# Kernel optimization log

Hardware: AMD Instinct MI355X
Metric: run time of the kernel (lower is better)

The kernel has to match this reference:

```python
import jax, jax.numpy as jnp
import numpy as np
import math

EPS = 1e-5
NUM_HEADS = 16


def _ln(x, g, b):
    m = jnp.mean(x, axis=-1, keepdims=True)
    v = jnp.mean(jnp.square(x - m), axis=-1, keepdims=True)
    return (x - m) * jax.lax.rsqrt(v + EPS) * g + b


def setup_inputs() -> dict:
    key = jax.random.key(0)
    ks = jax.random.split(key, 20)
    B, S, D = 16, 256, 1024
    G, L, QL = 576, 64, 16
    V = L * QL
    s = 0.02
    inp = {
        "hidden_states": jax.random.normal(ks[0], (B, S, D), jnp.float32),
        "global_ctx": jax.random.normal(ks[1], (B, G, D), jnp.float32),
        "vision_pos": jax.random.randint(ks[2], (B, G), 0, 1000),
        "instruct_pos": jax.random.randint(ks[3], (B, L), 0, 1000),
        "queries": jax.random.normal(ks[4], (B, V, D), jnp.float32),
        "image_tokens": jax.random.normal(ks[5], (B, V, D), jnp.float32),
        "query_len": QL,
        "W_in": jax.random.normal(ks[6], (D, 2 * D), jnp.float32) * s,
        "W_ctx": jax.random.normal(ks[7], (D, D), jnp.float32) * s,
        "ln_q_g": jnp.ones((D,), jnp.float32),
        "ln_q_b": jnp.zeros((D,), jnp.float32),
        "Wq": jax.random.normal(ks[8], (D, D), jnp.float32) * s,
        "ln_k_g": jnp.ones((D,), jnp.float32),
        "ln_k_b": jnp.zeros((D,), jnp.float32),
        "Wk": jax.random.normal(ks[9], (D, D), jnp.float32) * s,
        "ln_v_g": jnp.ones((D,), jnp.float32),
        "ln_v_b": jnp.zeros((D,), jnp.float32),
        "Wv": jax.random.normal(ks[10], (D, D), jnp.float32) * s,
        "Wo": jax.random.normal(ks[11], (D, D), jnp.float32) * s,
        "norm_g": jnp.ones((D,), jnp.float32),
        "norm_b": jnp.zeros((D,), jnp.float32),
        "W1": jax.random.normal(ks[12], (D, D), jnp.float32) * s,
        "W2": jax.random.normal(ks[13], (D, D), jnp.float32) * s,
    }
    return inp


def reference(hidden_states, global_ctx, vision_pos, instruct_pos, queries,
              image_tokens, query_len, W_in, W_ctx, ln_q_g, ln_q_b, Wq,
              ln_k_g, ln_k_b, Wk, ln_v_g, ln_v_b, Wv, Wo, norm_g, norm_b,
              W1, W2):
    B, V, _ = queries.shape
    D = hidden_states.shape[-1]
    G = global_ctx.shape[1]
    L = instruct_pos.shape[1]
    H = NUM_HEADS
    hd = D // H
    scale = 1.0 / math.sqrt(hd)
    Hq = int(math.sqrt(query_len))          # query grid side
    Hgc = int(math.sqrt(G))                 # ctx grid side
    Hw = Hgc // Hq                          # window side
    Wt = Hw * Hw                            # tokens per window

    residual = image_tokens
    # proj_in on concatenated queries
    pq = jnp.concatenate([queries, image_tokens], axis=-1) @ W_in.T  # (B,V,D)

    # window extraction: (B,Hgc,Wgc,D) -> (B, query_len, Wt, D)
    win = global_ctx.reshape(B, Hq, Hw, Hq, Hw, D)
    win = win.transpose(0, 1, 3, 2, 4, 5).reshape(B, query_len, Wt, D)
    win = win @ W_ctx.T                      # proj_context, shared across L

    # cross-attention: each query v attends only to window (v mod query_len)
    q = _ln(pq, ln_q_g, ln_q_b) @ Wq.T
    q = q.reshape(B, L, query_len, H, hd)
    k = (_ln(win, ln_k_g, ln_k_b) @ Wk.T).reshape(B, query_len, Wt, H, hd)
    v = (_ln(win, ln_v_g, ln_v_b) @ Wv.T).reshape(B, query_len, Wt, H, hd)

    scores = jnp.einsum('blqhd,bqwhd->blqhw', q, k) * scale
    attn = jax.nn.softmax(scores, axis=-1)
    ao = jnp.einsum('blqhw,bqwhd->blqhd', attn, v).reshape(B, V, D)
    ao = ao @ Wo.T

    x = _ln(ao + pq, norm_g, norm_b)
    out = jax.nn.gelu(x @ W1.T, approximate=False) @ W2.T
    return out + residual
```

## Files before the change

### kernel.cpp

```cpp
#include <hip/hip_runtime.h>
#include <cstdint>
#include <cstddef>

typedef unsigned short u16;
typedef __bf16 bf16_t;
typedef bf16_t bf16x8 __attribute__((ext_vector_type(8)));
typedef float f32x4 __attribute__((ext_vector_type(4)));

#define DEV __device__ __forceinline__
#define AS1 __attribute__((address_space(1)))
#define AS3 __attribute__((address_space(3)))

DEV u16 f2bf(float f) {
  unsigned u = __float_as_uint(f);
  u += 0x7fffu + ((u >> 16) & 1u);
  return (u16)(u >> 16);
}
DEV float bf2f(u16 h) {
  return __uint_as_float(((unsigned)h) << 16);
}

struct Cvt9 {
  const float* s[9];
  u16* d[9];
  long cumv[10];
};

__global__ __launch_bounds__(256)
void convert_batch(Cvt9 jobs) {
  const long total = jobs.cumv[9];
  for (long i = (long)blockIdx.x * 256 + threadIdx.x; i < total;
       i += (long)gridDim.x * 256) {
    int j = 0;
#pragma unroll
    for (int t = 0; t < 8; ++t)
      if (i >= jobs.cumv[t + 1]) j = t + 1;
    const long e = (i - jobs.cumv[j]) * 4;
    float4 v = *(const float4*)(jobs.s[j] + e);
    ushort4 o;
    o.x = f2bf(v.x); o.y = f2bf(v.y); o.z = f2bf(v.z); o.w = f2bf(v.w);
    *(ushort4*)(jobs.d[j] + e) = o;
  }
}

__global__ __launch_bounds__(256)
void build_acat(const float* __restrict__ q, const float* __restrict__ it,
                u16* __restrict__ dst) {
  const long total = 16384l * 2048 / 4;
  for (long i = (long)blockIdx.x * 256 + threadIdx.x; i < total;
       i += (long)gridDim.x * 256) {
    long e = i * 4;
    int m = (int)(e >> 11);
    int k = (int)(e & 2047);
    const float* s = (k < 1024) ? (q + (long)m * 1024 + k)
                                : (it + (long)m * 1024 + (k - 1024));
    float4 v = *(const float4*)s;
    ushort4 o;
    o.x = f2bf(v.x); o.y = f2bf(v.y); o.z = f2bf(v.z); o.w = f2bf(v.w);
    *(ushort4*)(dst + e) = o;
  }
}

__global__ __launch_bounds__(256)
void ln_rows(const float* __restrict__ x, const float* __restrict__ g,
             const float* __restrict__ b, u16* __restrict__ out) {
  __shared__ float red[8];
  const int row = blockIdx.x, tid = threadIdx.x;
  const float* xr = x + (size_t)row * 1024;
  float4 v = *(const float4*)(xr + tid * 4);
  float s = v.x + v.y + v.z + v.w;
  float ss = v.x * v.x + v.y * v.y + v.z * v.z + v.w * v.w;
#pragma unroll
  for (int o = 32; o > 0; o >>= 1) { s += __shfl_xor(s, o); ss += __shfl_xor(ss, o); }
  if ((tid & 63) == 0) { red[tid >> 6] = s; red[4 + (tid >> 6)] = ss; }
  __syncthreads();
  s = red[0] + red[1] + red[2] + red[3];
  ss = red[4] + red[5] + red[6] + red[7];
  const float mean = s * 0.0009765625f;
  const float var = ss * 0.0009765625f - mean * mean;
  const float rinv = rsqrtf(var + 1e-5f);
  const int c = tid * 4;
  float4 gg = *(const float4*)(g + c);
  float4 bb = *(const float4*)(b + c);
  ushort4 o4;
  o4.x = f2bf((v.x - mean) * rinv * gg.x + bb.x);
  o4.y = f2bf((v.y - mean) * rinv * gg.y + bb.y);
  o4.z = f2bf((v.z - mean) * rinv * gg.z + bb.z);
  o4.w = f2bf((v.w - mean) * rinv * gg.w + bb.w);
  *(ushort4*)(out + (size_t)row * 1024 + c) = o4;
}

__global__ __launch_bounds__(256)
void ln_kv(const float* __restrict__ winp,
           const float* __restrict__ gk, const float* __restrict__ bk,
           const float* __restrict__ gv, const float* __restrict__ bv,
           u16* __restrict__ kout, u16* __restrict__ vout) {
  __shared__ float red[8];
  const int m = blockIdx.x, tid = threadIdx.x;
  const int b = m / 576, rem = m % 576;
  const int qw = rem / 36, w = rem % 36;
  const int gidx = (qw >> 2) * 144 + (w / 6) * 24 + (qw & 3) * 6 + (w % 6);
  const float* xr = winp + ((size_t)b * 576 + gidx) * 1024;
  float4 v = *(const float4*)(xr + tid * 4);
  float s = v.x + v.y + v.z + v.w;
  float ss = v.x * v.x + v.y * v.y + v.z * v.z + v.w * v.w;
#pragma unroll
  for (int o = 32; o > 0; o >>= 1) { s += __shfl_xor(s, o); ss += __shfl_xor(ss, o); }
  if ((tid & 63) == 0) { red[tid >> 6] = s; red[4 + (tid >> 6)] = ss; }
  __syncthreads();
  s = red[0] + red[1] + red[2] + red[3];
  ss = red[4] + red[5] + red[6] + red[7];
  const float mean = s * 0.0009765625f;
  const float var = ss * 0.0009765625f - mean * mean;
  const float rinv = rsqrtf(var + 1e-5f);
  const int c = tid * 4;
  float4 gg = *(const float4*)(gk + c);
  float4 bb = *(const float4*)(bk + c);
  float4 g2 = *(const float4*)(gv + c);
  float4 b2 = *(const float4*)(bv + c);
  float nx = (v.x - mean) * rinv, ny = (v.y - mean) * rinv;
  float nz = (v.z - mean) * rinv, nw = (v.w - mean) * rinv;
  ushort4 ok, ov;
  ok.x = f2bf(nx * gg.x + bb.x); ok.y = f2bf(ny * gg.y + bb.y);
  ok.z = f2bf(nz * gg.z + bb.z); ok.w = f2bf(nw * gg.w + bb.w);
  ov.x = f2bf(nx * g2.x + b2.x); ov.y = f2bf(ny * g2.y + b2.y);
  ov.z = f2bf(nz * g2.z + b2.z); ov.w = f2bf(nw * g2.w + b2.w);
  *(ushort4*)(kout + (size_t)m * 1024 + c) = ok;
  *(ushort4*)(vout + (size_t)m * 1024 + c) = ov;
}

template <int EPI>
__global__ __launch_bounds__(512, 2)
void gemm256(const u16* __restrict__ A, const u16* __restrict__ Bw,
             u16* __restrict__ outB, float* __restrict__ outF,
             const float* __restrict__ addF, int M, int N, int K) {
  __shared__ __align__(16) u16 lds[2][2][16384];
  const int tid = threadIdx.x;
  const int wave = tid >> 6, lane = tid & 63;
  const int fr = lane & 15, fq = lane >> 4;
  const int swz = (blockIdx.x & 7) * ((int)gridDim.x >> 3) + (blockIdx.x >> 3);
  const int brow = (swz >> 2) << 8;
  const int bcol = (swz & 3) << 8;

  const int srow = tid >> 3;
  const int cgo = ((tid & 7) ^ (srow & 7)) << 3;
  const u16* pa0 = A + (size_t)(brow + srow) * K + cgo;
  const u16* pb0 = Bw + (size_t)(bcol + srow) * K + cgo;
  const size_t rstep = (size_t)64 * K;

  f32x4 acc[8][4];
#pragma unroll
  for (int mf = 0; mf < 8; ++mf)
#pragma unroll
    for (int nf = 0; nf < 4; ++nf) acc[mf][nf] = (f32x4){0.f, 0.f, 0.f, 0.f};

  const int fx = fr & 7;
  const int arow = (wave >> 2) * 128 + fr;
  const int brl = (wave & 3) * 64 + fr;

  auto STAGE_A = [&](int buf, int kt) {
    const int k0 = kt << 6;
#pragma unroll
    for (int i = 0; i < 4; ++i)
      __builtin_amdgcn_global_load_lds((const AS1 void*)(pa0 + i * rstep + k0),
                                       (AS3 void*)&lds[buf][0][i * 4096 + tid * 8],
                                       16, 0, 0);
  };
  auto STAGE_B = [&](int buf, int kt) {
    const int k0 = kt << 6;
#pragma unroll
    for (int i = 0; i < 4; ++i)
      __builtin_amdgcn_global_load_lds((const AS1 void*)(pb0 + i * rstep + k0),
                                       (AS3 void*)&lds[buf][1][i * 4096 + tid * 8],
                                       16, 0, 0);
  };

  const int NT = K >> 6;
  STAGE_A(0, 0);
  STAGE_B(0, 0);
  asm volatile("s_waitcnt vmcnt(0)" ::: "memory");
  __builtin_amdgcn_s_barrier();

  bf16x8 a[4], b[4];
  for (int t = 0; t < NT; ++t) {
    const u16* la = &lds[t & 1][0][0];
    const u16* lb = &lds[t & 1][1][0];
    const int nxt = (t + 1) & 1;

#pragma unroll
    for (int nf = 0; nf < 4; ++nf)
      b[nf] = *(const bf16x8*)&lb[(brl + nf * 16) * 64 + ((fq ^ fx) << 3)];
#pragma unroll
    for (int mf = 0; mf < 4; ++mf)
      a[mf] = *(const bf16x8*)&la[(arow + mf * 16) * 64 + ((fq ^ fx) << 3)];
    if (t + 1 < NT) STAGE_A(nxt, t + 1);
    __builtin_amdgcn_s_barrier();
    asm volatile("s_waitcnt lgkmcnt(0)" ::: "memory");
    __builtin_amdgcn_sched_barrier(0);
    __builtin_amdgcn_s_setprio(1);
#pragma unroll
    for (int mf = 0; mf < 4; ++mf)
#pragma unroll
      for (int nf = 0; nf < 4; ++nf)
        acc[mf][nf] = __builtin_amdgcn_mfma_f32_16x16x32_bf16(a[mf], b[nf],
                                                              acc[mf][nf], 0, 0, 0);
    __builtin_amdgcn_s_setprio(0);
    __builtin_amdgcn_s_barrier();

#pragma unroll
    for (int mf = 0; mf < 4; ++mf)
      a[mf] = *(const bf16x8*)&la[(arow + 64 + mf * 16) * 64 + ((fq ^ fx) << 3)];
    if (t + 1 < NT) STAGE_B(nxt, t + 1);
    __builtin_amdgcn_s_barrier();
    asm volatile("s_waitcnt lgkmcnt(0)" ::: "memory");
    __builtin_amdgcn_sched_barrier(0);
    __builtin_amdgcn_s_setprio(1);
#pragma unroll
    for (int mf = 0; mf < 4; ++mf)
#pragma unroll
      for (int nf = 0; nf < 4; ++nf)
        acc[4 + mf][nf] = __builtin_amdgcn_mfma_f32_16x16x32_bf16(a[mf], b[nf],
                                                                  acc[4 + mf][nf], 0, 0, 0);
    __builtin_amdgcn_s_setprio(0);
    __builtin_amdgcn_s_barrier();

#pragma unroll
    for (int nf = 0; nf < 4; ++nf)
      b[nf] = *(const bf16x8*)&lb[(brl + nf * 16) * 64 + (((4 + fq) ^ fx) << 3)];
#pragma unroll
    for (int mf = 0; mf < 4; ++mf)
      a[mf] = *(const bf16x8*)&la[(arow + mf * 16) * 64 + (((4 + fq) ^ fx) << 3)];
    __builtin_amdgcn_s_barrier();
    asm volatile("s_waitcnt lgkmcnt(0)" ::: "memory");
    __builtin_amdgcn_sched_barrier(0);
    __builtin_amdgcn_s_setprio(1);
#pragma unroll
    for (int mf = 0; mf < 4; ++mf)
#pragma unroll
      for (int nf = 0; nf < 4; ++nf)
        acc[mf][nf] = __builtin_amdgcn_mfma_f32_16x16x32_bf16(a[mf], b[nf],
                                                              acc[mf][nf], 0, 0, 0);
    __builtin_amdgcn_s_setprio(0);
    __builtin_amdgcn_s_barrier();

#pragma unroll
    for (int mf = 0; mf < 4; ++mf)
      a[mf] = *(const bf16x8*)&la[(arow + 64 + mf * 16) * 64 + (((4 + fq) ^ fx) << 3)];
    __builtin_amdgcn_s_barrier();
    asm volatile("s_waitcnt lgkmcnt(0)" ::: "memory");
    __builtin_amdgcn_sched_barrier(0);
    __builtin_amdgcn_s_setprio(1);
#pragma unroll
    for (int mf = 0; mf < 4; ++mf)
#pragma unroll
      for (int nf = 0; nf < 4; ++nf)
        acc[4 + mf][nf] = __builtin_amdgcn_mfma_f32_16x16x32_bf16(a[mf], b[nf],
                                                                  acc[4 + mf][nf], 0, 0, 0);
    __builtin_amdgcn_s_setprio(0);
    asm volatile("s_waitcnt vmcnt(0)" ::: "memory");
    __builtin_amdgcn_s_barrier();
  }

#pragma unroll
  for (int mf = 0; mf < 8; ++mf) {
    const int row0 = brow + (wave >> 2) * 128 + mf * 16 + fq * 4;
#pragma unroll
    for (int nf = 0; nf < 4; ++nf) {
      const int col = bcol + (wave & 3) * 64 + nf * 16 + fr;
#pragma unroll
      for (int j = 0; j < 4; ++j) {
        const size_t o = (size_t)(row0 + j) * N + col;
        const float vv = acc[mf][nf][j];
        if constexpr (EPI == 0) {
          outB[o] = f2bf(vv);
        } else if constexpr (EPI == 1) {
          outF[o] = vv;
        } else if constexpr (EPI == 2) {
          outF[o] = vv + addF[o];
        } else {
          outB[o] = f2bf(0.5f * vv * (1.0f + erff(vv * 0.70710678118654752f)));
        }
      }
    }
  }
}

__global__ __launch_bounds__(256)
void attn_kernel(const u16* __restrict__ q, const u16* __restrict__ k,
                 const u16* __restrict__ v, u16* __restrict__ ao) {
  __shared__ __align__(16) u16 Qs[64 * 64];
  __shared__ __align__(16) u16 Ks[36 * 64];
  __shared__ __align__(16) u16 Vs[36 * 64];
  __shared__ float Ps[64 * 36];
  const int bid = blockIdx.x;
  const int h = bid & 15, qw = (bid >> 4) & 15, b = bid >> 8;
  const int tid = threadIdx.x;
  const size_t qbase = ((size_t)b * 1024) * 1024 + (size_t)h * 64;
  for (int i = tid; i < 64 * 16; i += 256) {
    int l = i >> 4, d4 = (i & 15) * 4;
    *(ushort4*)&Qs[l * 64 + d4] =
        *(const ushort4*)&q[qbase + (size_t)(l * 16 + qw) * 1024 + d4];
  }
  const size_t kvbase = ((size_t)(b * 16 + qw)) * 36 * 1024 + (size_t)h * 64;
  for (int i = tid; i < 36 * 16; i += 256) {
    int w = i >> 4, d4 = (i & 15) * 4;
    *(ushort4*)&Ks[w * 64 + d4] = *(const ushort4*)&k[kvbase + (size_t)w * 1024 + d4];
    *(ushort4*)&Vs[w * 64 + d4] = *(const ushort4*)&v[kvbase + (size_t)w * 1024 + d4];
  }
  __syncthreads();
  const int l = tid >> 2, quad = tid & 3;
  float sc[9];
#pragma unroll
  for (int wi = 0; wi < 9; ++wi) {
    int w = quad * 9 + wi;
    float acc = 0.f;
#pragma unroll
    for (int dd = 0; dd < 64; dd += 4) {
      ushort4 qv = *(const ushort4*)&Qs[l * 64 + dd];
      ushort4 kv = *(const ushort4*)&Ks[w * 64 + dd];
      acc += bf2f(qv.x) * bf2f(kv.x) + bf2f(qv.y) * bf2f(kv.y) +
             bf2f(qv.z) * bf2f(kv.z) + bf2f(qv.w) * bf2f(kv.w);
    }
    sc[wi] = acc * 0.125f;
  }
  float mx = sc[0];
#pragma unroll
  for (int wi = 1; wi < 9; ++wi) mx = fmaxf(mx, sc[wi]);
  mx = fmaxf(mx, __shfl_xor(mx, 1));
  mx = fmaxf(mx, __shfl_xor(mx, 2));
  float sum = 0.f;
#pragma unroll
  for (int wi = 0; wi < 9; ++wi) { sc[wi] = __expf(sc[wi] - mx); sum += sc[wi]; }
  sum += __shfl_xor(sum, 1);
  sum += __shfl_xor(sum, 2);
  const float inv = 1.0f / sum;
#pragma unroll
  for (int wi = 0; wi < 9; ++wi) Ps[l * 36 + quad * 9 + wi] = sc[wi] * inv;
  __syncthreads();
  float o[16];
#pragma unroll
  for (int dd = 0; dd < 16; ++dd) o[dd] = 0.f;
  for (int w = 0; w < 36; ++w) {
    float p = Ps[l * 36 + w];
#pragma unroll
    for (int dd = 0; dd < 16; dd += 4) {
      ushort4 vv = *(const ushort4*)&Vs[w * 64 + quad * 16 + dd];
      o[dd] += p * bf2f(vv.x); o[dd + 1] += p * bf2f(vv.y);
      o[dd + 2] += p * bf2f(vv.z); o[dd + 3] += p * bf2f(vv.w);
    }
  }
  const size_t obase = qbase + (size_t)(l * 16 + qw) * 1024 + quad * 16;
#pragma unroll
  for (int dd = 0; dd < 16; dd += 4) {
    ushort4 ov;
    ov.x = f2bf(o[dd]); ov.y = f2bf(o[dd + 1]);
    ov.z = f2bf(o[dd + 2]); ov.w = f2bf(o[dd + 3]);
    *(ushort4*)&ao[obase + dd] = ov;
  }
}

extern "C" void kernel_launch(void* const* d_in, const int* in_sizes, int n_in,
                              void* d_out, int out_size, void* d_ws, size_t ws_size,
                              hipStream_t stream) {
  const float* gctx = (const float*)d_in[1];
  const float* queries = (const float*)d_in[4];
  const float* image_tokens = (const float*)d_in[5];
  const float* W_in = (const float*)d_in[7];
  const float* W_ctx = (const float*)d_in[8];
  const float* ln_q_g = (const float*)d_in[9];
  const float* ln_q_b = (const float*)d_in[10];
  const float* Wq = (const float*)d_in[11];
  const float* ln_k_g = (const float*)d_in[12];
  const float* ln_k_b = (const float*)d_in[13];
  const float* Wk = (const float*)d_in[14];
  const float* ln_v_g = (const float*)d_in[15];
  const float* ln_v_b = (const float*)d_in[16];
  const float* Wv = (const float*)d_in[17];
  const float* Wo = (const float*)d_in[18];
  const float* norm_g = (const float*)d_in[19];
  const float* norm_b = (const float*)d_in[20];
  const float* W1 = (const float*)d_in[21];
  const float* W2 = (const float*)d_in[22];
  float* out = (float*)d_out;

  char* ws = (char*)d_ws;
  const size_t MB = 1024 * 1024;
  u16* w_in_b  = (u16*)(ws + 0 * MB);
  u16* w_ctx_b = (u16*)(ws + 4 * MB);
  u16* wq_b    = (u16*)(ws + 6 * MB);
  u16* wk_b    = (u16*)(ws + 8 * MB);
  u16* wv_b    = (u16*)(ws + 10 * MB);
  u16* wo_b    = (u16*)(ws + 12 * MB);
  u16* w1_b    = (u16*)(ws + 14 * MB);
  u16* w2_b    = (u16*)(ws + 16 * MB);
  char* regA = ws + 18 * MB;
  char* regB = regA + 64 * MB;
  char* regC = regB + 36 * MB;

  u16* acat = (u16*)regA;
  u16* pqln = (u16*)regA;
  u16* qmat = (u16*)(regA + 32 * MB);
  u16* vln  = (u16*)regA;
  u16* aoh  = (u16*)regA;
  u16* xmat = (u16*)(regA + 32 * MB);

  float* winp = (float*)regB;
  u16* kmat = (u16*)regB;
  u16* vmat = (u16*)(regB + 18 * MB);
  u16* gout = (u16*)regB;

  u16* gcb = (u16*)regC;
  u16* kln = (u16*)regC;

  float* pq = out;

  Cvt9 jobs;
  const float* srcs[9] = {W_in, W_ctx, Wq, Wk, Wv, Wo, W1, W2, gctx};
  u16* dsts[9] = {w_in_b, w_ctx_b, wq_b, wk_b, wv_b, wo_b, w1_b, w2_b, gcb};
  long sizes[9] = {2048l * 1024, 1048576, 1048576, 1048576, 1048576,
                   1048576, 1048576, 1048576, 9216l * 1024};
  long cum = 0;
  for (int j = 0; j < 9; ++j) {
    jobs.s[j] = srcs[j];
    jobs.d[j] = dsts[j];
    jobs.cumv[j] = cum;
    cum += sizes[j] / 4;
  }
  jobs.cumv[9] = cum;
  convert_batch<<<dim3(2048), dim3(256), 0, stream>>>(jobs);
  build_acat<<<dim3(8192), dim3(256), 0, stream>>>(queries, image_tokens, acat);

  gemm256<1><<<dim3(256), dim3(512), 0, stream>>>(acat, w_in_b, nullptr, pq,
                                                  nullptr, 16384, 1024, 2048);
  ln_rows<<<dim3(16384), dim3(256), 0, stream>>>(pq, ln_q_g, ln_q_b, pqln);
  gemm256<0><<<dim3(256), dim3(512), 0, stream>>>(pqln, wq_b, qmat, nullptr,
                                                  nullptr, 16384, 1024, 1024);
  gemm256<1><<<dim3(144), dim3(512), 0, stream>>>(gcb, w_ctx_b, nullptr, winp,
                                                  nullptr, 9216, 1024, 1024);
  ln_kv<<<dim3(9216), dim3(256), 0, stream>>>(winp, ln_k_g, ln_k_b, ln_v_g,
                                              ln_v_b, kln, vln);
  gemm256<0><<<dim3(144), dim3(512), 0, stream>>>(kln, wk_b, kmat, nullptr,
                                                  nullptr, 9216, 1024, 1024);
  gemm256<0><<<dim3(144), dim3(512), 0, stream>>>(vln, wv_b, vmat, nullptr,
                                                  nullptr, 9216, 1024, 1024);
  attn_kernel<<<dim3(4096), dim3(256), 0, stream>>>(qmat, kmat, vmat, aoh);
  gemm256<2><<<dim3(256), dim3(512), 0, stream>>>(aoh, wo_b, nullptr, pq, pq,
                                                  16384, 1024, 1024);
  ln_rows<<<dim3(16384), dim3(256), 0, stream>>>(pq, norm_g, norm_b, xmat);
  gemm256<3><<<dim3(256), dim3(512), 0, stream>>>(xmat, w1_b, gout, nullptr,
                                                  nullptr, 16384, 1024, 1024);
  gemm256<2><<<dim3(256), dim3(512), 0, stream>>>(gout, w2_b, nullptr, out,
                                                  image_tokens, 16384, 1024, 1024);
}
```

Baseline: 531.8 us.

## Cut GEMM main-loop barriers and double-buffer A/B fragments in registers

The bf16 MFMA GEMM main loop is restructured. The many per-phase s_barrier and explicit lgkmcnt waits inside each K-tile iteration are removed, leaving a single __syncthreads at the end of the iteration. Separate register fragments (a0/a1, b0/b1) let the LDS reads for the next MFMA group be issued ahead of the current group, and the staging of the next tile is interleaved with compute. This is meant to cut barrier stalls and expose more overlap between LDS reads and MFMAs, at the cost of more VGPRs. Dropping the explicit vmcnt(0) means the LDS-DMA completion ordering now relies on the compiler's waitcnt insertion.

```diff
diff --git a/kernel.cpp b/kernel.cpp
--- a/kernel.cpp
+++ b/kernel.cpp
@@ -157,6 +157,8 @@
   const int fx = fr & 7;
   const int arow = (wave >> 2) * 128 + fr;
   const int brl = (wave & 3) * 64 + fr;
+  const int ck0 = (fq ^ fx) << 3;
+  const int ck1 = ((4 + fq) ^ fx) << 3;
 
   auto STAGE_A = [&](int buf, int kt) {
     const int k0 = kt << 6;
@@ -178,10 +180,9 @@
   const int NT = K >> 6;
   STAGE_A(0, 0);
   STAGE_B(0, 0);
-  asm volatile("s_waitcnt vmcnt(0)" ::: "memory");
-  __builtin_amdgcn_s_barrier();
-
-  bf16x8 a[4], b[4];
+  __syncthreads();
+
+  bf16x8 a0[4], a1[4], b0[4], b1[4];
   for (int t = 0; t < NT; ++t) {
     const u16* la = &lds[t & 1][0][0];
     const u16* lb = &lds[t & 1][1][0];
@@ -189,76 +190,61 @@
 
 #pragma unroll
     for (int nf = 0; nf < 4; ++nf)
-      b[nf] = *(const bf16x8*)&lb[(brl + nf * 16) * 64 + ((fq ^ fx) << 3)];
-#pragma unroll
-    for (int mf = 0; mf < 4; ++mf)
-      a[mf] = *(const bf16x8*)&la[(arow + mf * 16) * 64 + ((fq ^ fx) << 3)];
+      b0[nf] = *(const bf16x8*)&lb[(brl + nf * 16) * 64 + ck0];
+#pragma unroll
+    for (int mf = 0; mf < 4; ++mf)
+      a0[mf] = *(const bf16x8*)&la[(arow + mf * 16) * 64 + ck0];
+#pragma unroll
+    for (int mf = 0; mf < 4; ++mf)
+      a1[mf] = *(const bf16x8*)&la[(arow + 64 + mf * 16) * 64 + ck0];
     if (t + 1 < NT) STAGE_A(nxt, t + 1);
-    __builtin_amdgcn_s_barrier();
-    asm volatile("s_waitcnt lgkmcnt(0)" ::: "memory");
     __builtin_amdgcn_sched_barrier(0);
     __builtin_amdgcn_s_setprio(1);
 #pragma unroll
     for (int mf = 0; mf < 4; ++mf)
 #pragma unroll
       for (int nf = 0; nf < 4; ++nf)
-        acc[mf][nf] = __builtin_amdgcn_mfma_f32_16x16x32_bf16(a[mf], b[nf],
+        acc[mf][nf] = __builtin_amdgcn_mfma_f32_16x16x32_bf16(a0[mf], b0[nf],
                                                               acc[mf][nf], 0, 0, 0);
     __builtin_amdgcn_s_setprio(0);
-    __builtin_amdgcn_s_barrier();
-
-#pragma unroll
-    for (int mf = 0; mf < 4; ++mf)
-      a[mf] = *(const bf16x8*)&la[(arow + 64 + mf * 16) * 64 + ((fq ^ fx) << 3)];
-    if (t + 1 < NT) STAGE_B(nxt, t + 1);
-    __builtin_amdgcn_s_barrier();
-    asm volatile("s_waitcnt lgkmcnt(0)" ::: "memory");
+#pragma unroll
+    for (int nf = 0; nf < 4; ++nf)
+      b1[nf] = *(const bf16x8*)&lb[(brl + nf * 16) * 64 + ck1];
+#pragma unroll
+    for (int mf = 0; mf < 4; ++mf)
+      a0[mf] = *(const bf16x8*)&la[(arow + mf * 16) * 64 + ck1];
     __builtin_amdgcn_sched_barrier(0);
     __builtin_amdgcn_s_setprio(1);
 #pragma unroll
     for (int mf = 0; mf < 4; ++mf)
 #pragma unroll
       for (int nf = 0; nf < 4; ++nf)
-        acc[4 + mf][nf] = __builtin_amdgcn_mfma_f32_16x16x32_bf16(a[mf], b[nf],
+        acc[4 + mf][nf] = __builtin_amdgcn_mfma_f32_16x16x32_bf16(a1[mf], b0[nf],
                                                                   acc[4 + mf][nf], 0, 0, 0);
     __builtin_amdgcn_s_setprio(0);
-    __builtin_amdgcn_s_barrier();
-
-#pragma unroll
-    for (int nf = 0; nf < 4; ++nf)
-      b[nf] = *(const bf16x8*)&lb[(brl + nf * 16) * 64 + (((4 + fq) ^ fx) << 3)];
-#pragma unroll
-    for (int mf = 0; mf < 4; ++mf)
-      a[mf] = *(const bf16x8*)&la[(arow + mf * 16) * 64 + (((4 + fq) ^ fx) << 3)];
-    __builtin_amdgcn_s_barrier();
-    asm volatile("s_waitcnt lgkmcnt(0)" ::: "memory");
+#pragma unroll
+    for (int mf = 0; mf < 4; ++mf)
+      a1[mf] = *(const bf16x8*)&la[(arow + 64 + mf * 16) * 64 + ck1];
+    if (t + 1 < NT) STAGE_B(nxt, t + 1);
     __builtin_amdgcn_sched_barrier(0);
     __builtin_amdgcn_s_setprio(1);
 #pragma unroll
     for (int mf = 0; mf < 4; ++mf)
 #pragma unroll
       for (int nf = 0; nf < 4; ++nf)
-        acc[mf][nf] = __builtin_amdgcn_mfma_f32_16x16x32_bf16(a[mf], b[nf],
+        acc[mf][nf] = __builtin_amdgcn_mfma_f32_16x16x32_bf16(a0[mf], b1[nf],
                                                               acc[mf][nf], 0, 0, 0);
     __builtin_amdgcn_s_setprio(0);
-    __builtin_amdgcn_s_barrier();
-
-#pragma unroll
-    for (int mf = 0; mf < 4; ++mf)
-      a[mf] = *(const bf16x8*)&la[(arow + 64 + mf * 16) * 64 + (((4 + fq) ^ fx) << 3)];
-    __builtin_amdgcn_s_barrier();
-    asm volatile("s_waitcnt lgkmcnt(0)" ::: "memory");
     __builtin_amdgcn_sched_barrier(0);
     __builtin_amdgcn_s_setprio(1);
 #pragma unroll
     for (int mf = 0; mf < 4; ++mf)
 #pragma unroll
       for (int nf = 0; nf < 4; ++nf)
-        acc[4 + mf][nf] = __builtin_amdgcn_mfma_f32_16x16x32_bf16(a[mf], b[nf],
+        acc[4 + mf][nf] = __builtin_amdgcn_mfma_f32_16x16x32_bf16(a1[mf], b1[nf],
                                                                   acc[4 + mf][nf], 0, 0, 0);
     __builtin_amdgcn_s_setprio(0);
-    asm volatile("s_waitcnt vmcnt(0)" ::: "memory");
-    __builtin_amdgcn_s_barrier();
+    __syncthreads();
   }
 
 #pragma unroll
```

New measurement: 522.0 us. Within noise of the previous version (-1.9%).
